# Kernel optimization log

Hardware: AMD Instinct MI355X
Metric: run time of the kernel (lower is better)

The kernel has to match this reference:

```python
import jax, jax.numpy as jnp
import numpy as np

PIECES = 64  # self.plane


def _proj(f, w1, b1, w2, b2):
    # Projection: fc2(relu(fc1(f))), final_relu=False
    h = jax.nn.relu(f @ w1 + b1)
    return h @ w2 + b2


def _cf(img, param, pieces):
    # img: [B,3,H,W], param: [B,3,P]
    # total[b,c,h,w] = sum_i clamp(img - i/P, 0, 1/P) * param[b,c,i], then * P / sum_i param
    grid = jnp.arange(pieces, dtype=img.dtype) / pieces            # [P]
    clipped = jnp.clip(img[..., None] - grid, 0.0, 1.0 / pieces)   # [B,3,H,W,P]
    total = jnp.einsum('bchwp,bcp->bchw', clipped, param)
    norm = pieces / (jnp.sum(param, axis=-1) + 1e-30)              # [B,3]
    return total * norm[:, :, None, None]


def setup_inputs() -> dict:
    key = jax.random.key(0)
    ks = jax.random.split(key, 11)
    B, H, W = 8, 256, 256
    s = 0.05
    return {
        'x': jax.random.uniform(ks[0], (B, 3, H, W), jnp.float32),
        'f_feature': jax.random.normal(ks[1], (B, 512), jnp.float32),
        'b_feature': jax.random.normal(ks[2], (B, 512), jnp.float32),
        # stacked weights for [fc_f_1, fc_b_1, fc_f_s, fc_b_s]
        'proj_w1': jax.random.normal(ks[3], (4, 512, 192), jnp.float32) * s,
        'proj_b1': jax.random.normal(ks[4], (4, 192), jnp.float32) * s,
        'proj_w2': jax.random.normal(ks[5], (4, 192, 192), jnp.float32) * s,
        'proj_b2': jax.random.normal(ks[6], (4, 192), jnp.float32) * s,
        'fc_w1': jax.random.normal(ks[7], (576, 192), jnp.float32) * s,
        'fc_b1': jax.random.normal(ks[8], (192,), jnp.float32) * s,
        'fc_w2': jax.random.normal(ks[9], (192, 192), jnp.float32) * s,
        'fc_b2': jax.random.normal(ks[10], (192,), jnp.float32) * s,
    }


def reference(x, f_feature, b_feature, proj_w1, proj_b1, proj_w2, proj_b2,
              fc_w1, fc_b1, fc_w2, fc_b2):
    B = x.shape[0]
    # rgb_to_grayscale with 3 output channels (ITU-R 601 weights)
    gw = jnp.array([0.299, 0.587, 0.114], dtype=x.dtype)
    gray = jnp.broadcast_to(jnp.einsum('bchw,c->bhw', x, gw)[:, None], x.shape)

    # four stacked Projections: inputs [f, b, f, b]
    feats = jnp.stack([f_feature, b_feature, f_feature, b_feature])       # [4,B,512]
    h = jax.nn.relu(jnp.einsum('kbi,kio->kbo', feats, proj_w1) + proj_b1[:, None, :])
    outs = jnp.einsum('kbo,koq->kbq', h, proj_w2) + proj_b2[:, None, :]   # [4,B,192]
    param_f, param_b = outs[0], outs[1]
    param_s = outs[2] + outs[3]

    cat = jnp.concatenate([param_f, param_b, param_s], axis=1)            # [B,576]
    param = _proj(cat, fc_w1, fc_b1, fc_w2, fc_b2)                        # [B,192]

    p_all = param.reshape(B, 3, PIECES)
    p_f = param_f.reshape(B, 3, PIECES)
    p_b = param_b.reshape(B, 3, PIECES)

    return (_cf(x, p_all, PIECES), _cf(gray, p_f, PIECES), _cf(gray, p_b, PIECES))
```

## Files before the change

### kernel.cpp

```cpp
#include <hip/hip_runtime.h>

#define HWSZ 65536
#define PLANE (3 * HWSZ)
#define OUTSTRIDE (8 * PLANE)
#define MAGIC 0x13572468

__global__ __launch_bounds__(384) void k_mlp(
    const float* __restrict__ f, const float* __restrict__ bf,
    const float* __restrict__ pw1, const float* __restrict__ pb1,
    const float* __restrict__ pw2, const float* __restrict__ pb2,
    const float* __restrict__ fw1, const float* __restrict__ fb1,
    const float* __restrict__ fw2, const float* __restrict__ fb2,
    float* __restrict__ ws) {
  __shared__ float smem[2304];
  int t = threadIdx.x, blk = blockIdx.x;

  float* outs  = ws;
  float* param = ws + 6144;
  int* flags = (int*)(ws + 8192);

  int k = blk >> 3, b = blk & 7;
  int q = t % 48, s = t / 48;
  {
    float* sf  = smem;
    float* red = smem + 512;
    float* sh  = smem + 2048;

    const float* feat = ((k & 1) ? bf : f) + b * 512;
    for (int i = t; i < 512; i += 384) sf[i] = feat[i];
    __syncthreads();

    {
      const float4* w = (const float4*)(pw1 + (size_t)k * (512 * 192));
      float4 acc = {0.f, 0.f, 0.f, 0.f};
      int i0 = s * 64;
      for (int r = 0; r < 4; ++r) {
        float4 wv[16];
#pragma unroll
        for (int j = 0; j < 16; ++j)
          wv[j] = w[(size_t)(i0 + r * 16 + j) * 48 + q];
#pragma unroll
        for (int j = 0; j < 16; ++j) {
          float v = sf[i0 + r * 16 + j];
          acc.x = fmaf(v, wv[j].x, acc.x); acc.y = fmaf(v, wv[j].y, acc.y);
          acc.z = fmaf(v, wv[j].z, acc.z); acc.w = fmaf(v, wv[j].w, acc.w);
        }
      }
      ((float4*)(red + s * 192))[q] = acc;
    }
    __syncthreads();
    if (t < 192) {
      float a = pb1[k * 192 + t];
#pragma unroll
      for (int s2 = 0; s2 < 8; ++s2) a += red[s2 * 192 + t];
      sh[t] = fmaxf(a, 0.f);
    }
    __syncthreads();
    {
      const float4* w = (const float4*)(pw2 + (size_t)k * (192 * 192));
      float4 acc = {0.f, 0.f, 0.f, 0.f};
      int i0 = s * 24;
      for (int r = 0; r < 2; ++r) {
        float4 wv[12];
#pragma unroll
        for (int j = 0; j < 12; ++j)
          wv[j] = w[(size_t)(i0 + r * 12 + j) * 48 + q];
#pragma unroll
        for (int j = 0; j < 12; ++j) {
          float v = sh[i0 + r * 12 + j];
          acc.x = fmaf(v, wv[j].x, acc.x); acc.y = fmaf(v, wv[j].y, acc.y);
          acc.z = fmaf(v, wv[j].z, acc.z); acc.w = fmaf(v, wv[j].w, acc.w);
        }
      }
      ((float4*)(red + s * 192))[q] = acc;
    }
    __syncthreads();
    if (t < 192) {
      float a = pb2[k * 192 + t];
#pragma unroll
      for (int s2 = 0; s2 < 8; ++s2) a += red[s2 * 192 + t];
      outs[(k * 8 + b) * 192 + t] = a;
    }
    __syncthreads();
    if (t == 0) {
      __threadfence();
      atomicExch(&flags[(k * 8 + b) * 16], MAGIC);
    }
  }

  if (blk >= 8) return;

  int b2 = blk;
  if (t < 4) {
    while (atomicAdd(&flags[(t * 8 + b2) * 16], 0) != MAGIC)
      __builtin_amdgcn_s_sleep(2);
  }
  __syncthreads();
  if (t == 0) __threadfence();
  __syncthreads();

  float* sc   = smem;
  float* redb = smem + 576;
  float* shb  = smem + 2112;
  for (int idx = t; idx < 576; idx += 384) {
    float v;
    if (idx < 192)      v = outs[(0 * 8 + b2) * 192 + idx];
    else if (idx < 384) v = outs[(1 * 8 + b2) * 192 + (idx - 192)];
    else                v = outs[(2 * 8 + b2) * 192 + (idx - 384)] +
                            outs[(3 * 8 + b2) * 192 + (idx - 384)];
    sc[idx] = v;
  }
  __syncthreads();
  {
    const float4* w = (const float4*)fw1;
    float4 acc = {0.f, 0.f, 0.f, 0.f};
    int i0 = s * 72;
    for (int r = 0; r < 4; ++r) {
      float4 wv[18];
#pragma unroll
      for (int j = 0; j < 18; ++j)
        wv[j] = w[(size_t)(i0 + r * 18 + j) * 48 + q];
#pragma unroll
      for (int j = 0; j < 18; ++j) {
        float v = sc[i0 + r * 18 + j];
        acc.x = fmaf(v, wv[j].x, acc.x); acc.y = fmaf(v, wv[j].y, acc.y);
        acc.z = fmaf(v, wv[j].z, acc.z); acc.w = fmaf(v, wv[j].w, acc.w);
      }
    }
    ((float4*)(redb + s * 192))[q] = acc;
  }
  __syncthreads();
  if (t < 192) {
    float a = fb1[t];
#pragma unroll
    for (int s2 = 0; s2 < 8; ++s2) a += redb[s2 * 192 + t];
    shb[t] = fmaxf(a, 0.f);
  }
  __syncthreads();
  {
    const float4* w = (const float4*)fw2;
    float4 acc = {0.f, 0.f, 0.f, 0.f};
    int i0 = s * 24;
    for (int r = 0; r < 2; ++r) {
      float4 wv[12];
#pragma unroll
      for (int j = 0; j < 12; ++j)
        wv[j] = w[(size_t)(i0 + r * 12 + j) * 48 + q];
#pragma unroll
      for (int j = 0; j < 12; ++j) {
        float v = shb[i0 + r * 12 + j];
        acc.x = fmaf(v, wv[j].x, acc.x); acc.y = fmaf(v, wv[j].y, acc.y);
        acc.z = fmaf(v, wv[j].z, acc.z); acc.w = fmaf(v, wv[j].w, acc.w);
      }
    }
    ((float4*)(redb + s * 192))[q] = acc;
  }
  __syncthreads();
  if (t < 192) {
    float a = fb2[t];
#pragma unroll
    for (int s2 = 0; s2 < 8; ++s2) a += redb[s2 * 192 + t];
    param[b2 * 192 + t] = a;
  }
}

__global__ __launch_bounds__(256) void k_render(
    const float* __restrict__ x, const float* __restrict__ ws,
    float* __restrict__ out) {
  int b = blockIdx.y, t = threadIdx.x;
  int wave = t >> 6, lane = t & 63;
  const float* outs  = ws;
  const float* param = ws + 6144;
  __shared__ float2 tab[576];

  for (int cur = wave; cur < 9; cur += 4) {
    int oi = cur / 3, c = cur - oi * 3;
    const float* src = (oi == 0) ? param + b * 192 + c * 64
                                 : outs + ((oi - 1) * 8 + b) * 192 + c * 64;
    float p = src[lane];
    float v = p;
#pragma unroll
    for (int d = 1; d < 64; d <<= 1) {
      float n = __shfl_up(v, d, 64);
      if (lane >= d) v += n;
    }
    float total = __shfl(v, 63, 64);
    float norm = 64.f / (total + 1e-30f);
    tab[cur * 64 + lane] = make_float2((v - p) * 0.015625f * norm, p * norm);
  }
  __syncthreads();

  auto ev = [&](int cur, float v) -> float {
    int k = (int)(v * 64.f);
    k = k < 0 ? 0 : (k > 63 ? 63 : k);
    float2 e = tab[cur * 64 + k];
    float tt = v - (float)k * 0.015625f;
    return fmaf(tt, e.y, e.x);
  };
  auto ev4 = [&](int cur, float4 v) -> float4 {
    float4 r;
    r.x = ev(cur, v.x); r.y = ev(cur, v.y);
    r.z = ev(cur, v.z); r.w = ev(cur, v.w);
    return r;
  };

  int s4 = blockIdx.x * 256 + t;
  const float* xb = x + (size_t)b * PLANE;
  float4 vr = ((const float4*)(xb))[s4];
  float4 vg = ((const float4*)(xb + HWSZ))[s4];
  float4 vb = ((const float4*)(xb + 2 * HWSZ))[s4];

  float4 gr;
  gr.x = fmaf(0.299f, vr.x, fmaf(0.587f, vg.x, 0.114f * vb.x));
  gr.y = fmaf(0.299f, vr.y, fmaf(0.587f, vg.y, 0.114f * vb.y));
  gr.z = fmaf(0.299f, vr.z, fmaf(0.587f, vg.z, 0.114f * vb.z));
  gr.w = fmaf(0.299f, vr.w, fmaf(0.587f, vg.w, 0.114f * vb.w));

  float* o0 = out + (size_t)b * PLANE;
  float* o1 = out + OUTSTRIDE + (size_t)b * PLANE;
  float* o2 = out + 2 * OUTSTRIDE + (size_t)b * PLANE;

  ((float4*)(o0))[s4]            = ev4(0, vr);
  ((float4*)(o0 + HWSZ))[s4]     = ev4(1, vg);
  ((float4*)(o0 + 2 * HWSZ))[s4] = ev4(2, vb);
  ((float4*)(o1))[s4]            = ev4(3, gr);
  ((float4*)(o1 + HWSZ))[s4]     = ev4(4, gr);
  ((float4*)(o1 + 2 * HWSZ))[s4] = ev4(5, gr);
  ((float4*)(o2))[s4]            = ev4(6, gr);
  ((float4*)(o2 + HWSZ))[s4]     = ev4(7, gr);
  ((float4*)(o2 + 2 * HWSZ))[s4] = ev4(8, gr);
}

extern "C" void kernel_launch(void* const* d_in, const int* in_sizes, int n_in,
                              void* d_out, int out_size, void* d_ws, size_t ws_size,
                              hipStream_t stream) {
  const float* x   = (const float*)d_in[0];
  const float* f   = (const float*)d_in[1];
  const float* bf  = (const float*)d_in[2];
  const float* pw1 = (const float*)d_in[3];
  const float* pb1 = (const float*)d_in[4];
  const float* pw2 = (const float*)d_in[5];
  const float* pb2 = (const float*)d_in[6];
  const float* fw1 = (const float*)d_in[7];
  const float* fb1 = (const float*)d_in[8];
  const float* fw2 = (const float*)d_in[9];
  const float* fb2 = (const float*)d_in[10];
  float* out = (float*)d_out;
  float* ws  = (float*)d_ws;

  k_mlp<<<32, 384, 0, stream>>>(f, bf, pw1, pb1, pw2, pb2, fw1, fb1, fw2,
                                fb2, ws);
  dim3 grid(64, 8);
  k_render<<<grid, 256, 0, stream>>>(x, ws, out);
}
```

Before: 101.8 us.

## Split second-stage MLP across all 32 blocks and prefetch image before table build

The fusion MLP (fc1 and fc2 on the concatenated params) previously ran on only 8 blocks, one per batch element. It is now split by output column chunks across all 32 blocks, with an extra flag barrier through workspace between fc1 and fc2. In the render kernel, the image loads are issued before the parameter prefix-sum table is built, so global load latency overlaps the table work. The cost is an additional inter-block spin-wait, which relies on all 32 blocks being co-resident.

```diff
diff --git a/kernel.cpp b/kernel.cpp
--- a/kernel.cpp
+++ b/kernel.cpp
@@ -16,12 +16,13 @@
   int t = threadIdx.x, blk = blockIdx.x;
 
   float* outs  = ws;
-  float* param = ws + 6144;
-  int* flags = (int*)(ws + 8192);
+  float* hc    = ws + 12288;
+  float* param = ws + 13824;
+  int* fbase = (int*)(ws + 16384);
 
   int k = blk >> 3, b = blk & 7;
-  int q = t % 48, s = t / 48;
   {
+    int q = t % 48, s = t / 48;
     float* sf  = smem;
     float* red = smem + 512;
     float* sh  = smem + 2048;
@@ -84,83 +85,99 @@
     __syncthreads();
     if (t == 0) {
       __threadfence();
-      atomicExch(&flags[(k * 8 + b) * 16], MAGIC);
-    }
-  }
-
-  if (blk >= 8) return;
-
-  int b2 = blk;
+      atomicExch(&fbase[blk * 16], MAGIC);
+    }
+  }
+
+  int b2 = blk & 7, c4 = blk >> 3, ob2 = c4 * 48;
   if (t < 4) {
-    while (atomicAdd(&flags[(t * 8 + b2) * 16], 0) != MAGIC)
+    while (atomicAdd(&fbase[(t * 8 + b2) * 16], 0) != MAGIC)
       __builtin_amdgcn_s_sleep(2);
   }
   __syncthreads();
   if (t == 0) __threadfence();
   __syncthreads();
 
-  float* sc   = smem;
-  float* redb = smem + 576;
-  float* shb  = smem + 2112;
-  for (int idx = t; idx < 576; idx += 384) {
-    float v;
-    if (idx < 192)      v = outs[(0 * 8 + b2) * 192 + idx];
-    else if (idx < 384) v = outs[(1 * 8 + b2) * 192 + (idx - 192)];
-    else                v = outs[(2 * 8 + b2) * 192 + (idx - 384)] +
-                            outs[(3 * 8 + b2) * 192 + (idx - 384)];
-    sc[idx] = v;
-  }
-  __syncthreads();
   {
+    int q = t % 12, s = t / 12;
+    float* sc  = smem;
+    float* red = smem + 576;
+    for (int idx = t; idx < 576; idx += 384) {
+      float v;
+      if (idx < 192)      v = outs[(0 * 8 + b2) * 192 + idx];
+      else if (idx < 384) v = outs[(1 * 8 + b2) * 192 + (idx - 192)];
+      else                v = outs[(2 * 8 + b2) * 192 + (idx - 384)] +
+                              outs[(3 * 8 + b2) * 192 + (idx - 384)];
+      sc[idx] = v;
+    }
     const float4* w = (const float4*)fw1;
     float4 acc = {0.f, 0.f, 0.f, 0.f};
-    int i0 = s * 72;
-    for (int r = 0; r < 4; ++r) {
+    int i0 = s * 18;
+    {
       float4 wv[18];
 #pragma unroll
       for (int j = 0; j < 18; ++j)
-        wv[j] = w[(size_t)(i0 + r * 18 + j) * 48 + q];
+        wv[j] = w[(size_t)(i0 + j) * 48 + (ob2 >> 2) + q];
+      __syncthreads();
 #pragma unroll
       for (int j = 0; j < 18; ++j) {
-        float v = sc[i0 + r * 18 + j];
+        float v = sc[i0 + j];
         acc.x = fmaf(v, wv[j].x, acc.x); acc.y = fmaf(v, wv[j].y, acc.y);
         acc.z = fmaf(v, wv[j].z, acc.z); acc.w = fmaf(v, wv[j].w, acc.w);
       }
     }
-    ((float4*)(redb + s * 192))[q] = acc;
-  }
-  __syncthreads();
-  if (t < 192) {
-    float a = fb1[t];
-#pragma unroll
-    for (int s2 = 0; s2 < 8; ++s2) a += redb[s2 * 192 + t];
-    shb[t] = fmaxf(a, 0.f);
-  }
-  __syncthreads();
+    ((float4*)(red + s * 48))[q] = acc;
+    __syncthreads();
+    if (t < 48) {
+      float a = fb1[ob2 + t];
+#pragma unroll
+      for (int s2 = 0; s2 < 32; ++s2) a += red[s2 * 48 + t];
+      hc[b2 * 192 + ob2 + t] = fmaxf(a, 0.f);
+    }
+    __syncthreads();
+    if (t == 0) {
+      __threadfence();
+      atomicExch(&fbase[(64 + blk) * 16], MAGIC);
+    }
+  }
+
+  if (t < 4) {
+    while (atomicAdd(&fbase[(64 + t * 8 + b2) * 16], 0) != MAGIC)
+      __builtin_amdgcn_s_sleep(2);
+  }
+  __syncthreads();
+  if (t == 0) __threadfence();
+  __syncthreads();
+
   {
+    int q = t % 12, s = t / 12;
+    float* sh  = smem;
+    float* red = smem + 576;
+    if (t < 192) sh[t] = hc[b2 * 192 + t];
     const float4* w = (const float4*)fw2;
     float4 acc = {0.f, 0.f, 0.f, 0.f};
-    int i0 = s * 24;
-    for (int r = 0; r < 2; ++r) {
-      float4 wv[12];
-#pragma unroll
-      for (int j = 0; j < 12; ++j)
-        wv[j] = w[(size_t)(i0 + r * 12 + j) * 48 + q];
-#pragma unroll
-      for (int j = 0; j < 12; ++j) {
-        float v = shb[i0 + r * 12 + j];
+    int i0 = s * 6;
+    {
+      float4 wv[6];
+#pragma unroll
+      for (int j = 0; j < 6; ++j)
+        wv[j] = w[(size_t)(i0 + j) * 48 + (ob2 >> 2) + q];
+      __syncthreads();
+#pragma unroll
+      for (int j = 0; j < 6; ++j) {
+        float v = sh[i0 + j];
         acc.x = fmaf(v, wv[j].x, acc.x); acc.y = fmaf(v, wv[j].y, acc.y);
         acc.z = fmaf(v, wv[j].z, acc.z); acc.w = fmaf(v, wv[j].w, acc.w);
       }
     }
-    ((float4*)(redb + s * 192))[q] = acc;
-  }
-  __syncthreads();
-  if (t < 192) {
-    float a = fb2[t];
-#pragma unroll
-    for (int s2 = 0; s2 < 8; ++s2) a += redb[s2 * 192 + t];
-    param[b2 * 192 + t] = a;
+    ((float4*)(red + s * 48))[q] = acc;
+    __syncthreads();
+    if (t < 48) {
+      float a = fb2[ob2 + t];
+#pragma unroll
+      for (int s2 = 0; s2 < 32; ++s2) a += red[s2 * 48 + t];
+      param[b2 * 192 + ob2 + t] = a;
+    }
   }
 }
 
@@ -170,8 +187,14 @@
   int b = blockIdx.y, t = threadIdx.x;
   int wave = t >> 6, lane = t & 63;
   const float* outs  = ws;
-  const float* param = ws + 6144;
+  const float* param = ws + 13824;
   __shared__ float2 tab[576];
+
+  int s4 = blockIdx.x * 256 + t;
+  const float* xb = x + (size_t)b * PLANE;
+  float4 vr = ((const float4*)(xb))[s4];
+  float4 vg = ((const float4*)(xb + HWSZ))[s4];
+  float4 vb = ((const float4*)(xb + 2 * HWSZ))[s4];
 
   for (int cur = wave; cur < 9; cur += 4) {
     int oi = cur / 3, c = cur - oi * 3;
@@ -203,12 +226,6 @@
     r.z = ev(cur, v.z); r.w = ev(cur, v.w);
     return r;
   };
-
-  int s4 = blockIdx.x * 256 + t;
-  const float* xb = x + (size_t)b * PLANE;
-  float4 vr = ((const float4*)(xb))[s4];
-  float4 vg = ((const float4*)(xb + HWSZ))[s4];
-  float4 vb = ((const float4*)(xb + 2 * HWSZ))[s4];
 
   float4 gr;
   gr.x = fmaf(0.299f, vr.x, fmaf(0.587f, vg.x, 0.114f * vb.x));
```

Result: no change. 100.1 us (-1.7%).
